# Performance work log

Hardware: AMD Instinct MI355X
Metric: run time of the kernel (lower is better)

The kernel has to match this reference:

```python
import jax, jax.numpy as jnp
import numpy as np

N_NODES = 16384   # total nodes
B = 32            # graphs in batch
NPG = 512         # nodes per graph (uniform -> dense mask is all True)
E = 262144        # edges (avg degree 16)
H = 64            # hidden_dim
HEADS = 8
DH = H // HEADS


def setup_inputs() -> dict:
    key = jax.random.key(0)
    ks = jax.random.split(key, 20)
    x = jax.random.normal(ks[0], (N_NODES, H), dtype=jnp.float32)
    # edges constrained within each graph of 512 nodes
    src = jax.random.randint(ks[1], (E,), 0, N_NODES, dtype=jnp.int32)
    dst = (src // NPG) * NPG + jax.random.randint(ks[2], (E,), 0, NPG, dtype=jnp.int32)
    edge_index = jnp.stack([src, dst])
    batch = (jnp.arange(N_NODES, dtype=jnp.int32) // NPG)
    c_size = jnp.full((B,), NPG, dtype=jnp.int32)
    s = 1.0 / np.sqrt(H)
    p = lambda k, shape: (jax.random.normal(k, shape, dtype=jnp.float32) * s)
    return {
        "x": x,
        "w_gat": p(ks[3], (H, H)), "att_src": p(ks[4], (H,)), "att_dst": p(ks[5], (H,)), "b_gat": jnp.zeros((H,), jnp.float32),
        "g1": jnp.ones((H,), jnp.float32), "b1": jnp.zeros((H,), jnp.float32),
        "wq": p(ks[6], (H, H)), "bq": jnp.zeros((H,), jnp.float32),
        "wk": p(ks[7], (H, H)), "bk": jnp.zeros((H,), jnp.float32),
        "wv": p(ks[8], (H, H)), "bv": jnp.zeros((H,), jnp.float32),
        "wo": p(ks[9], (H, H)), "bo": jnp.zeros((H,), jnp.float32),
        "g2": jnp.ones((H,), jnp.float32), "b2": jnp.zeros((H,), jnp.float32),
        "edge_index": edge_index, "batch": batch, "c_size": c_size,
    }


def _layer_norm(x, g, b):
    mu = jnp.mean(x, axis=-1, keepdims=True)
    var = jnp.var(x, axis=-1, keepdims=True)
    return (x - mu) * jax.lax.rsqrt(var + 1e-5) * g + b


def _gat_conv(x, edge_index, w, a_src, a_dst, bias):
    # PyG GATConv, 1 head, add_self_loops=True, leaky_relu slope 0.2
    n = x.shape[0]
    loops = jnp.arange(n, dtype=edge_index.dtype)
    src = jnp.concatenate([edge_index[0], loops])
    dst = jnp.concatenate([edge_index[1], loops])
    h = x @ w                                  # [n, H]
    e = jax.nn.leaky_relu((h @ a_src)[src] + (h @ a_dst)[dst], 0.2)  # [E+n]
    m = jax.ops.segment_max(e, dst, num_segments=n)
    p = jnp.exp(e - m[dst])
    s = jax.ops.segment_sum(p, dst, num_segments=n)
    alpha = p / (s[dst] + 1e-16)
    out = jax.ops.segment_sum(alpha[:, None] * h[src], dst, num_segments=n)
    return out + bias


def reference(x, w_gat, att_src, att_dst, b_gat, g1, b1,
              wq, bq, wk, bk, wv, bv, wo, bo, g2, b2,
              edge_index, batch, c_size):
    # GAT branch (dropout is identity in eval)
    x_ = jax.nn.relu(_gat_conv(x, edge_index, w_gat, att_src, att_dst, b_gat))
    x1 = _layer_norm(x + x_, g1, b1)                     # [n, H]
    # to_dense_batch: uniform graphs -> mask all True, plain reshape
    xd = x1.reshape(B, NPG, H)
    q = (xd @ wq + bq).reshape(B, NPG, HEADS, DH)
    k = (xd @ wk + bk).reshape(B, NPG, HEADS, DH)
    v = (xd @ wv + bv).reshape(B, NPG, HEADS, DH)
    scores = jnp.einsum('bqhd,bkhd->bhqk', q, k) / np.sqrt(DH)  # [B,h,N,N]
    attn = jax.nn.softmax(scores, axis=-1)
    o = jnp.einsum('bhqk,bkhd->bqhd', attn, v).reshape(B, NPG, H)
    o = o @ wo + bo
    x2 = _layer_norm(x1 + jax.nn.relu(o.reshape(N_NODES, H)), g2, b2)
    return x2  # recon_loss is None in eval mode
```

## Files before the change

### kernel.cpp

```cpp
#include <hip/hip_runtime.h>
#include <hip/hip_bf16.h>

#define NN     16384
#define HD     64
#define BG     32
#define NPG    512
#define NHEADS 8
#define DH     8
#define DEGMAX 40

#define KVSTR  20
#define CSTR   (64 * KVSTR + 4)

typedef __hip_bfloat16 bf16;

#if defined(__has_builtin)
#if __has_builtin(__builtin_amdgcn_exp2f)
#define EXP2F(x) __builtin_amdgcn_exp2f(x)
#else
#define EXP2F(x) exp2f(x)
#endif
#else
#define EXP2F(x) exp2f(x)
#endif

__device__ __forceinline__ float b2f(bf16 v) { return __bfloat162float(v); }

__device__ __forceinline__ float ldf(const void* p, int i, int bf) {
  return bf ? __bfloat162float(((const bf16*)p)[i]) : ((const float*)p)[i];
}

__device__ __forceinline__ float wave_sum(float v) {
#pragma unroll
  for (int off = 32; off > 0; off >>= 1) v += __shfl_xor(v, off);
  return v;
}

__device__ __forceinline__ void unpack8(uint4 u, float* f) {
  f[0] = __uint_as_float(u.x << 16); f[1] = __uint_as_float(u.x & 0xffff0000u);
  f[2] = __uint_as_float(u.y << 16); f[3] = __uint_as_float(u.y & 0xffff0000u);
  f[4] = __uint_as_float(u.z << 16); f[5] = __uint_as_float(u.z & 0xffff0000u);
  f[6] = __uint_as_float(u.w << 16); f[7] = __uint_as_float(u.w & 0xffff0000u);
}

__device__ __forceinline__ unsigned short bfbits(float f) {
  bf16 b = __float2bfloat16(f);
  return *(unsigned short*)&b;
}

__device__ __forceinline__ int detect_bf(const unsigned short* xr, int tid, int nt) {
  __shared__ int s_cnt;
  if (tid == 0) s_cnt = 0;
  __syncthreads();
  int sane = 0;
  for (int i = tid; i < 256; i += nt) {
    int e = (xr[2 * i] >> 7) & 0xFF;
    sane += (e >= 100 && e <= 150) ? 1 : 0;
  }
  if (sane) atomicAdd(&s_cnt, sane);
  __syncthreads();
  return s_cnt > 180;
}

__global__ __launch_bounds__(256) void k_build(
    const void* __restrict__ x, const void* __restrict__ w,
    const void* __restrict__ asrc, const void* __restrict__ adst,
    const int* __restrict__ esrc, const int* __restrict__ edst, int E,
    int* __restrict__ cur, int* __restrict__ ell,
    bf16* __restrict__ h, float* __restrict__ as_, float* __restrict__ ad_,
    int* __restrict__ flagp)
{
  const int tid = threadIdx.x, lane = tid & 63, wid = tid >> 6;
  const int bf = detect_bf((const unsigned short*)x, tid, 256);
  if (tid == 0 && blockIdx.x == 0) *flagp = bf;
  __shared__ float wl[HD * HD];
  __shared__ float xr[4][HD];
  {
    for (int e = blockIdx.x * 256 + tid; e < E; e += gridDim.x * 256) {
      int d = edst[e];
      int k = atomicAdd(&cur[d], 1);
      if (k < DEGMAX) ell[d * DEGMAX + k] = esrc[e];
    }
  }
  for (int i = tid; i < HD * HD; i += 256) wl[i] = ldf(w, i, bf);
  const float av = ldf(asrc, lane, bf), dv_ = ldf(adst, lane, bf);
  __syncthreads();
#pragma unroll
  for (int r = 0; r < 4; ++r) {
    const int node = blockIdx.x * 16 + r * 4 + wid;
    xr[wid][lane] = ldf(x, node * HD + lane, bf);
    float hj = 0.f;
#pragma unroll
    for (int i = 0; i < HD; ++i) hj = fmaf(xr[wid][i], wl[i * HD + lane], hj);
    float pa = wave_sum(hj * av);
    float pd = wave_sum(hj * dv_);
    h[node * HD + lane] = __float2bfloat16(hj);
    if (lane == 0) { as_[node] = pa; ad_[node] = pd; }
  }
}

__global__ __launch_bounds__(256) void k_gather(
    const void* __restrict__ x, const int* __restrict__ cur,
    const int* __restrict__ ell, const float* __restrict__ as_,
    const float* __restrict__ ad_, const bf16* __restrict__ h,
    const void* __restrict__ bg, const void* __restrict__ g1,
    const void* __restrict__ b1, const int* __restrict__ dflag,
    bf16* __restrict__ x1)
{
  const int tid = threadIdx.x, lane = tid & 63, wid = tid >> 6;
  const int bf = *dflag;
  const int n = blockIdx.x * 4 + wid;
  const float adn = ad_[n];
  float e0 = as_[n] + adn;
  e0 = e0 > 0.f ? e0 : 0.2f * e0;
  float den = __expf(fminf(e0, 30.f));
  float num = den * b2f(h[n * HD + lane]);
  const int deg = min(cur[n], DEGMAX);
  const int* row = ell + n * DEGMAX;
  int i = 0;
  for (; i + 8 <= deg; i += 8) {
    int s[8];
#pragma unroll
    for (int k = 0; k < 8; ++k) s[k] = row[i + k];
    float a[8], hh[8];
#pragma unroll
    for (int k = 0; k < 8; ++k) a[k] = as_[s[k]];
#pragma unroll
    for (int k = 0; k < 8; ++k) hh[k] = b2f(h[s[k] * HD + lane]);
#pragma unroll
    for (int k = 0; k < 8; ++k) {
      float e = a[k] + adn;
      e = e > 0.f ? e : 0.2f * e;
      float p = __expf(fminf(e, 30.f));
      den += p;
      num = fmaf(p, hh[k], num);
    }
  }
  for (; i + 4 <= deg; i += 4) {
    int s0 = row[i], s1 = row[i + 1], s2 = row[i + 2], s3 = row[i + 3];
    float a0 = as_[s0], a1 = as_[s1], a2 = as_[s2], a3 = as_[s3];
    float h0 = b2f(h[s0 * HD + lane]), h1 = b2f(h[s1 * HD + lane]);
    float h2 = b2f(h[s2 * HD + lane]), h3 = b2f(h[s3 * HD + lane]);
    float e_0 = a0 + adn; e_0 = e_0 > 0.f ? e_0 : 0.2f * e_0;
    float e_1 = a1 + adn; e_1 = e_1 > 0.f ? e_1 : 0.2f * e_1;
    float e_2 = a2 + adn; e_2 = e_2 > 0.f ? e_2 : 0.2f * e_2;
    float e_3 = a3 + adn; e_3 = e_3 > 0.f ? e_3 : 0.2f * e_3;
    float p0 = __expf(fminf(e_0, 30.f)), p1 = __expf(fminf(e_1, 30.f));
    float p2 = __expf(fminf(e_2, 30.f)), p3 = __expf(fminf(e_3, 30.f));
    den += p0 + p1 + p2 + p3;
    num = fmaf(p0, h0, num); num = fmaf(p1, h1, num);
    num = fmaf(p2, h2, num); num = fmaf(p3, h3, num);
  }
  for (; i < deg; ++i) {
    int s = row[i];
    float e = as_[s] + adn;
    e = e > 0.f ? e : 0.2f * e;
    float p = __expf(fminf(e, 30.f));
    den += p;
    num = fmaf(p, b2f(h[s * HD + lane]), num);
  }
  float v = num / (den + 1e-16f) + ldf(bg, lane, bf);
  v = fmaxf(v, 0.f) + ldf(x, n * HD + lane, bf);
  float mu = wave_sum(v) * (1.f / 64.f);
  float dv = v - mu;
  float var = wave_sum(dv * dv) * (1.f / 64.f);
  float r = rsqrtf(var + 1e-5f);
  x1[n * HD + lane] =
      __float2bfloat16(dv * r * ldf(g1, lane, bf) + ldf(b1, lane, bf));
}

__global__ __launch_bounds__(512, 4) void k_attn13(
    const bf16* __restrict__ x1,
    const void* __restrict__ wq, const void* __restrict__ bq,
    const void* __restrict__ wk, const void* __restrict__ bk,
    const void* __restrict__ wv, const void* __restrict__ bv,
    const int* __restrict__ dflag,
    bf16* __restrict__ num_t, float* __restrict__ den_t)
{
  const int t = threadIdx.x;
  const int bf = *dflag;
  __shared__ float KV[4 * CSTR];
  __shared__ float Wl[3][HD][DH];
  __shared__ float bl[3][DH];
  const int bid = blockIdx.x;
  const int g = bid >> 4, hd = (bid >> 1) & 7, half = bid & 1;
  {
    int i = t >> 3, j = t & 7;
    int col = hd * DH + j;
    Wl[0][i][j] = ldf(wq, i * HD + col, bf);
    Wl[1][i][j] = ldf(wk, i * HD + col, bf);
    Wl[2][i][j] = ldf(wv, i * HD + col, bf);
    if (t < DH) {
      bl[0][t] = ldf(bq, hd * DH + t, bf);
      bl[1][t] = ldf(bk, hd * DH + t, bf);
      bl[2][t] = ldf(bv, hd * DH + t, bf);
    }
  }
  __syncthreads();
  const float qscale = 0.3535533905932738f * 1.4426950408889634f;
  {
    const int r = t & 255;
    const int m = (t < 256) ? 1 : 2;
    const uint4* xk4 = (const uint4*)(x1 + (size_t)(g * NPG + half * 256 + r) * HD);
    float acc[DH];
#pragma unroll
    for (int j = 0; j < DH; ++j) acc[j] = bl[m][j];
#pragma unroll
    for (int blk = 0; blk < 8; ++blk) {
      float xv[8];
      unpack8(xk4[blk], xv);
      const int ib = blk * 8;
#pragma unroll
      for (int ii = 0; ii < 8; ++ii)
#pragma unroll
        for (int j = 0; j < DH; ++j)
          acc[j] = fmaf(xv[ii], Wl[m][ib + ii][j], acc[j]);
    }
    float* kvrow = KV + (r >> 6) * CSTR + (r & 63) * KVSTR + (t < 256 ? 0 : 8);
    *(float4*)(kvrow + 0) = make_float4(acc[0], acc[1], acc[2], acc[3]);
    *(float4*)(kvrow + 4) = make_float4(acc[4], acc[5], acc[6], acc[7]);
  }
  float qa[DH];
  {
    const uint4* xa4 = (const uint4*)(x1 + (size_t)(g * NPG + t) * HD);
#pragma unroll
    for (int j = 0; j < DH; ++j) qa[j] = bl[0][j];
#pragma unroll
    for (int blk = 0; blk < 8; ++blk) {
      float xv[8];
      unpack8(xa4[blk], xv);
      const int ib = blk * 8;
#pragma unroll
      for (int ii = 0; ii < 8; ++ii)
#pragma unroll
        for (int j = 0; j < DH; ++j)
          qa[j] = fmaf(xv[ii], Wl[0][ib + ii][j], qa[j]);
    }
#pragma unroll
    for (int j = 0; j < DH; ++j) qa[j] *= qscale;
  }
  __syncthreads();
  const int lane = t & 63;
  const int base = lane & ~3;
  float qv[4][DH];
#pragma unroll
  for (int i = 0; i < 4; ++i)
#pragma unroll
    for (int j = 0; j < DH; ++j)
      qv[i][j] = __shfl(qa[j], base + i, 64);
  const int qg = t >> 2, c = t & 3;
  float den[4], num[4][DH];
#pragma unroll
  for (int i = 0; i < 4; ++i) {
    den[i] = 0.f;
#pragma unroll
    for (int j = 0; j < DH; ++j) num[i][j] = 0.f;
  }
  const float* kvc = KV + c * CSTR;
#pragma unroll 4
  for (int jj = 0; jj < 64; ++jj) {
    const float4* kv4 = (const float4*)(kvc + jj * KVSTR);
    float4 k0 = kv4[0], k1 = kv4[1], v0 = kv4[2], v1 = kv4[3];
#pragma unroll
    for (int i = 0; i < 4; ++i) {
      float s = qv[i][0] * k0.x;
      s = fmaf(qv[i][1], k0.y, s); s = fmaf(qv[i][2], k0.z, s);
      s = fmaf(qv[i][3], k0.w, s); s = fmaf(qv[i][4], k1.x, s);
      s = fmaf(qv[i][5], k1.y, s); s = fmaf(qv[i][6], k1.z, s);
      s = fmaf(qv[i][7], k1.w, s);
      float p = EXP2F(s);
      den[i] += p;
      num[i][0] = fmaf(p, v0.x, num[i][0]); num[i][1] = fmaf(p, v0.y, num[i][1]);
      num[i][2] = fmaf(p, v0.z, num[i][2]); num[i][3] = fmaf(p, v0.w, num[i][3]);
      num[i][4] = fmaf(p, v1.x, num[i][4]); num[i][5] = fmaf(p, v1.y, num[i][5]);
      num[i][6] = fmaf(p, v1.z, num[i][6]); num[i][7] = fmaf(p, v1.w, num[i][7]);
    }
  }
#pragma unroll
  for (int st = 1; st <= 2; st <<= 1) {
#pragma unroll
    for (int i = 0; i < 4; ++i) {
      den[i] += __shfl_xor(den[i], st);
#pragma unroll
      for (int j = 0; j < DH; ++j) num[i][j] += __shfl_xor(num[i][j], st);
    }
  }
  const int plane = half * 8 + hd;
  float dsel = 0.f, rsel[DH];
#pragma unroll
  for (int j = 0; j < DH; ++j) rsel[j] = 0.f;
#pragma unroll
  for (int i = 0; i < 4; ++i) {
    if (c == i) {
      dsel = den[i];
#pragma unroll
      for (int j = 0; j < DH; ++j) rsel[j] = num[i][j];
    }
  }
  const int qrow = qg * 4 + c;
  union { uint4 u4; unsigned short us[8]; } pk;
#pragma unroll
  for (int j = 0; j < DH; ++j) pk.us[j] = bfbits(rsel[j]);
  *(uint4*)(num_t + ((size_t)plane * NN + g * NPG + qrow) * 8) = pk.u4;
  den_t[(size_t)plane * NN + g * NPG + qrow] = dsel;
}

__global__ __launch_bounds__(256) void k_out(
    const bf16* __restrict__ num_t, const float* __restrict__ den_t,
    const bf16* __restrict__ x1,
    const void* __restrict__ wo, const void* __restrict__ bo,
    const void* __restrict__ g2, const void* __restrict__ b2,
    const int* __restrict__ dflag, void* __restrict__ out)
{
  const int tid = threadIdx.x, lane = tid & 63, wid = tid >> 6;
  const int bf = *dflag;
  __shared__ float wl[HD * HD];
  __shared__ float orow[4][HD];
  for (int i = tid; i < HD * HD; i += 256) wl[i] = ldf(wo, i, bf);
  const float bov = ldf(bo, lane, bf);
  const float g2v = ldf(g2, lane, bf);
  const float b2v = ldf(b2, lane, bf);
  const int hdp = lane >> 3, jp = lane & 7;
  __syncthreads();
#pragma unroll
  for (int r = 0; r < 8; ++r) {
    const int node = blockIdx.x * 32 + r * 4 + wid;
    {
      float nm = b2f(num_t[((size_t)hdp * NN + node) * 8 + jp]) +
                 b2f(num_t[((size_t)(8 + hdp) * NN + node) * 8 + jp]);
      float dn = den_t[(size_t)hdp * NN + node] +
                 den_t[(size_t)(8 + hdp) * NN + node];
      orow[wid][lane] = nm / dn;
    }
    float y = bov;
#pragma unroll
    for (int i = 0; i < HD; ++i) y = fmaf(orow[wid][i], wl[i * HD + lane], y);
    float tt = b2f(x1[node * HD + lane]) + fmaxf(y, 0.f);
    float mu = wave_sum(tt) * (1.f / 64.f);
    float dv = tt - mu;
    float var = wave_sum(dv * dv) * (1.f / 64.f);
    float rr = rsqrtf(var + 1e-5f);
    float res = dv * rr * g2v + b2v;
    if (bf) ((bf16*)out)[node * HD + lane] = __float2bfloat16(res);
    else    ((float*)out)[node * HD + lane] = res;
  }
}

extern "C" void kernel_launch(void* const* d_in, const int* in_sizes, int n_in,
                              void* d_out, int out_size, void* d_ws, size_t ws_size,
                              hipStream_t stream)
{
  const void* x    = d_in[0];
  const void* wgat = d_in[1];
  const void* asrc = d_in[2];
  const void* adst = d_in[3];
  const void* bgat = d_in[4];
  const void* g1   = d_in[5];
  const void* b1   = d_in[6];
  const void* wq   = d_in[7];
  const void* bq   = d_in[8];
  const void* wk   = d_in[9];
  const void* bk   = d_in[10];
  const void* wv   = d_in[11];
  const void* bv   = d_in[12];
  const void* wo   = d_in[13];
  const void* bo   = d_in[14];
  const void* g2   = d_in[15];
  const void* b2   = d_in[16];
  const int*  ei   = (const int*)d_in[17];
  const int E = in_sizes[17] / 2;
  const int* esrc = ei;
  const int* edst = ei + E;

  char* W = (char*)d_ws;
  bf16*  x1b   = (bf16*)W;
  int*   ell   = (int*)(W + (size_t)(2 << 20));
  bf16*  hb    = (bf16*)(W + (size_t)(2 << 20) + (size_t)NN * DEGMAX * 4);
  bf16*  num_t = (bf16*)(W + (size_t)(2 << 20));
  float* den_t = (float*)(W + (size_t)(6 << 20));
  float* as_   = (float*)(W + (size_t)(7 << 20));
  float* ad_   = as_ + NN;
  int*   cur   = (int*)(ad_ + NN);
  int*   flag  = cur + NN;

  hipMemsetAsync(cur, 0, NN * sizeof(int), stream);
  k_build  <<<NN / 16, 256, 0, stream>>>(x, wgat, asrc, adst, esrc, edst, E,
                                         cur, ell, hb, as_, ad_, flag);
  k_gather <<<NN / 4, 256, 0, stream>>>(x, cur, ell, as_, ad_, hb,
                                        bgat, g1, b1, flag, x1b);
  k_attn13 <<<BG * NHEADS * 2, 512, 0, stream>>>(x1b, wq, bq, wk, bk, wv, bv,
                                                 flag, num_t, den_t);
  k_out    <<<NN / 32, 256, 0, stream>>>(num_t, den_t, x1b, wo, bo, g2, b2,
                                         flag, d_out);
}
```

Before: 194.9 us.

## Compute attention scores and PV products with fp16 MFMA instructions

The attention kernel now stores Q, K and transposed V as fp16 in shared memory and uses 32x32x8 f16 MFMA instructions for both QK^T and P·V, in place of scalar FMA loops over fp32 K/V tiles. Exponentials are packed to fp16 and fed straight back into the second MFMA. The occupancy hint drops from 4 to 2 blocks. The aim is to move most attention FLOPs onto matrix cores, at the cost of fp16 precision for scores and probabilities, which could overflow if logits grow, plus wasted MFMA columns because DH=8 fills only 8 of 32 output columns.

```diff
diff --git a/kernel.cpp b/kernel.cpp
--- a/kernel.cpp
+++ b/kernel.cpp
@@ -1,5 +1,6 @@
 #include <hip/hip_runtime.h>
 #include <hip/hip_bf16.h>
+#include <hip/hip_fp16.h>
 
 #define NN     16384
 #define HD     64
@@ -9,10 +10,13 @@
 #define DH     8
 #define DEGMAX 40
 
-#define KVSTR  20
-#define CSTR   (64 * KVSTR + 4)
+#define QS_STR 12
+#define KS_STR 12
+#define VT_STR 264
 
 typedef __hip_bfloat16 bf16;
+typedef _Float16 v4h __attribute__((ext_vector_type(4)));
+typedef float v16f __attribute__((ext_vector_type(16)));
 
 #if defined(__has_builtin)
 #if __has_builtin(__builtin_amdgcn_exp2f)
@@ -46,6 +50,12 @@
 __device__ __forceinline__ unsigned short bfbits(float f) {
   bf16 b = __float2bfloat16(f);
   return *(unsigned short*)&b;
+}
+
+__device__ __forceinline__ unsigned packh2(float a, float b) {
+  union { unsigned u; __half2 h; } z;
+  z.h = __floats2half2_rn(a, b);
+  return z.u;
 }
 
 __device__ __forceinline__ int detect_bf(const unsigned short* xr, int tid, int nt) {
@@ -169,7 +179,7 @@
       __float2bfloat16(dv * r * ldf(g1, lane, bf) + ldf(b1, lane, bf));
 }
 
-__global__ __launch_bounds__(512, 4) void k_attn13(
+__global__ __launch_bounds__(512, 2) void k_attn13(
     const bf16* __restrict__ x1,
     const void* __restrict__ wq, const void* __restrict__ bq,
     const void* __restrict__ wk, const void* __restrict__ bk,
@@ -179,7 +189,9 @@
 {
   const int t = threadIdx.x;
   const int bf = *dflag;
-  __shared__ float KV[4 * CSTR];
+  __shared__ _Float16 Qs[NPG * QS_STR];
+  __shared__ _Float16 Ks[256 * KS_STR];
+  __shared__ _Float16 Vt[DH * VT_STR];
   __shared__ float Wl[3][HD][DH];
   __shared__ float bl[3][DH];
   const int bid = blockIdx.x;
@@ -216,13 +228,19 @@
         for (int j = 0; j < DH; ++j)
           acc[j] = fmaf(xv[ii], Wl[m][ib + ii][j], acc[j]);
     }
-    float* kvrow = KV + (r >> 6) * CSTR + (r & 63) * KVSTR + (t < 256 ? 0 : 8);
-    *(float4*)(kvrow + 0) = make_float4(acc[0], acc[1], acc[2], acc[3]);
-    *(float4*)(kvrow + 4) = make_float4(acc[4], acc[5], acc[6], acc[7]);
-  }
-  float qa[DH];
+    if (t < 256) {
+      unsigned w0 = packh2(acc[0], acc[1]), w1 = packh2(acc[2], acc[3]);
+      unsigned w2 = packh2(acc[4], acc[5]), w3 = packh2(acc[6], acc[7]);
+      *(uint2*)(Ks + r * KS_STR) = make_uint2(w0, w1);
+      *(uint2*)(Ks + r * KS_STR + 4) = make_uint2(w2, w3);
+    } else {
+#pragma unroll
+      for (int j = 0; j < DH; ++j) Vt[j * VT_STR + r] = (_Float16)acc[j];
+    }
+  }
   {
     const uint4* xa4 = (const uint4*)(x1 + (size_t)(g * NPG + t) * HD);
+    float qa[DH];
 #pragma unroll
     for (int j = 0; j < DH; ++j) qa[j] = bl[0][j];
 #pragma unroll
@@ -236,73 +254,54 @@
         for (int j = 0; j < DH; ++j)
           qa[j] = fmaf(xv[ii], Wl[0][ib + ii][j], qa[j]);
     }
-#pragma unroll
-    for (int j = 0; j < DH; ++j) qa[j] *= qscale;
-  }
-  __syncthreads();
-  const int lane = t & 63;
-  const int base = lane & ~3;
-  float qv[4][DH];
-#pragma unroll
-  for (int i = 0; i < 4; ++i)
-#pragma unroll
-    for (int j = 0; j < DH; ++j)
-      qv[i][j] = __shfl(qa[j], base + i, 64);
-  const int qg = t >> 2, c = t & 3;
-  float den[4], num[4][DH];
-#pragma unroll
-  for (int i = 0; i < 4; ++i) {
-    den[i] = 0.f;
-#pragma unroll
-    for (int j = 0; j < DH; ++j) num[i][j] = 0.f;
-  }
-  const float* kvc = KV + c * CSTR;
-#pragma unroll 4
-  for (int jj = 0; jj < 64; ++jj) {
-    const float4* kv4 = (const float4*)(kvc + jj * KVSTR);
-    float4 k0 = kv4[0], k1 = kv4[1], v0 = kv4[2], v1 = kv4[3];
-#pragma unroll
-    for (int i = 0; i < 4; ++i) {
-      float s = qv[i][0] * k0.x;
-      s = fmaf(qv[i][1], k0.y, s); s = fmaf(qv[i][2], k0.z, s);
-      s = fmaf(qv[i][3], k0.w, s); s = fmaf(qv[i][4], k1.x, s);
-      s = fmaf(qv[i][5], k1.y, s); s = fmaf(qv[i][6], k1.z, s);
-      s = fmaf(qv[i][7], k1.w, s);
-      float p = EXP2F(s);
-      den[i] += p;
-      num[i][0] = fmaf(p, v0.x, num[i][0]); num[i][1] = fmaf(p, v0.y, num[i][1]);
-      num[i][2] = fmaf(p, v0.z, num[i][2]); num[i][3] = fmaf(p, v0.w, num[i][3]);
-      num[i][4] = fmaf(p, v1.x, num[i][4]); num[i][5] = fmaf(p, v1.y, num[i][5]);
-      num[i][6] = fmaf(p, v1.z, num[i][6]); num[i][7] = fmaf(p, v1.w, num[i][7]);
-    }
-  }
-#pragma unroll
-  for (int st = 1; st <= 2; st <<= 1) {
-#pragma unroll
-    for (int i = 0; i < 4; ++i) {
-      den[i] += __shfl_xor(den[i], st);
-#pragma unroll
-      for (int j = 0; j < DH; ++j) num[i][j] += __shfl_xor(num[i][j], st);
-    }
-  }
+    unsigned w0 = packh2(qa[0] * qscale, qa[1] * qscale);
+    unsigned w1 = packh2(qa[2] * qscale, qa[3] * qscale);
+    unsigned w2 = packh2(qa[4] * qscale, qa[5] * qscale);
+    unsigned w3 = packh2(qa[6] * qscale, qa[7] * qscale);
+    *(uint2*)(Qs + t * QS_STR) = make_uint2(w0, w1);
+    *(uint2*)(Qs + t * QS_STR + 4) = make_uint2(w2, w3);
+  }
+  __syncthreads();
+  const int lane = t & 63, wid = t >> 6;
+  const int ln = lane & 31, hh = lane >> 5;
   const int plane = half * 8 + hd;
-  float dsel = 0.f, rsel[DH];
-#pragma unroll
-  for (int j = 0; j < DH; ++j) rsel[j] = 0.f;
-#pragma unroll
-  for (int i = 0; i < 4; ++i) {
-    if (c == i) {
-      dsel = den[i];
-#pragma unroll
-      for (int j = 0; j < DH; ++j) rsel[j] = num[i][j];
-    }
-  }
-  const int qrow = qg * 4 + c;
-  union { uint4 u4; unsigned short us[8]; } pk;
-#pragma unroll
-  for (int j = 0; j < DH; ++j) pk.us[j] = bfbits(rsel[j]);
-  *(uint4*)(num_t + ((size_t)plane * NN + g * NPG + qrow) * 8) = pk.u4;
-  den_t[(size_t)plane * NN + g * NPG + qrow] = dsel;
+  const size_t obase = (size_t)plane * NN + (size_t)g * NPG;
+  v16f zf;
+#pragma unroll
+  for (int i = 0; i < 16; ++i) zf[i] = 0.f;
+#pragma unroll
+  for (int qt = 0; qt < 2; ++qt) {
+    const int qbase = (wid * 2 + qt) * 32;
+    v4h qf = *(const v4h*)(Qs + (qbase + ln) * QS_STR + 4 * hh);
+    v16f oacc = zf;
+    float den = 0.f;
+#pragma unroll
+    for (int kt = 0; kt < 8; ++kt) {
+      v4h kf = *(const v4h*)(Ks + (kt * 32 + ln) * KS_STR + 4 * hh);
+      v16f s = __builtin_amdgcn_mfma_f32_32x32x8f16(kf, qf, zf, 0, 0, 0);
+#pragma unroll
+      for (int g2 = 0; g2 < 4; ++g2) {
+        float e0 = EXP2F(s[4 * g2 + 0]);
+        float e1 = EXP2F(s[4 * g2 + 1]);
+        float e2 = EXP2F(s[4 * g2 + 2]);
+        float e3 = EXP2F(s[4 * g2 + 3]);
+        den += (e0 + e1) + (e2 + e3);
+        union { unsigned u[2]; v4h v; } pu;
+        pu.u[0] = packh2(e0, e1);
+        pu.u[1] = packh2(e2, e3);
+        v4h vf = *(const v4h*)(Vt + (ln & 7) * VT_STR + kt * 32 + g2 * 8 + 4 * hh);
+        oacc = __builtin_amdgcn_mfma_f32_32x32x8f16(pu.v, vf, oacc, 0, 0, 0);
+      }
+    }
+    den += __shfl_xor(den, 32);
+    if (lane < 32) den_t[obase + qbase + lane] = den;
+#pragma unroll
+    for (int r = 0; r < 16; ++r) {
+      const int q = qbase + (r & 3) + 8 * (r >> 2) + 4 * hh;
+      if (ln < 8)
+        num_t[(obase + q) * 8 + ln] = __float2bfloat16(oacc[r]);
+    }
+  }
 }
 
 __global__ __launch_bounds__(256) void k_out(
```

Measured after the change: 178.7 us. 8.3% less time.
